# Kernel tuning notes

Measured on AMD Instinct MI355X. Metric: run time of the kernel, lower is better.

## Reference

```python
import jax, jax.numpy as jnp
import numpy as np

DIM = 2048
HEADS = 16
DIM_HEAD = 128
FF_MULT = 4
ATTN_INNER = HEADS * DIM_HEAD            # 2048
FF_INNER = DIM * FF_MULT                 # 8192
FUSED = ATTN_INNER + DIM_HEAD + DIM_HEAD + 2 * FF_INNER  # 18688
B, N = 2, 2048


def setup_inputs() -> dict:
    key = jax.random.key(0)
    k0, k1, k2, k3 = jax.random.split(key, 4)
    s = lambda fan_in: 1.0 / np.sqrt(fan_in)
    return {
        "x": jax.random.normal(k0, (B, N, DIM), jnp.float32),
        "gamma": jnp.ones((DIM,), jnp.float32),
        "beta": jnp.zeros((DIM,), jnp.float32),
        "w_fused": jax.random.normal(k1, (DIM, FUSED), jnp.float32) * s(DIM),
        "w_attn_out": jax.random.normal(k2, (ATTN_INNER, DIM), jnp.float32) * s(ATTN_INNER),
        "w_ff_out": jax.random.normal(k3, (FF_INNER, DIM), jnp.float32) * s(FF_INNER),
    }


def _rotate_half(t):
    t1, t2 = jnp.split(t, 2, axis=-1)
    return jnp.concatenate([-t2, t1], axis=-1)


def _rope(pos, t):
    # pos: [n, d] broadcast over leading dims of t (..., n, d)
    return t * jnp.cos(pos) + _rotate_half(t) * jnp.sin(pos)


def reference(x, gamma, beta, w_fused, w_attn_out, w_ff_out):
    b, n, d = x.shape
    # LayerNorm (eps = 1e-5, matching F.layer_norm default)
    mu = jnp.mean(x, axis=-1, keepdims=True)
    var = jnp.var(x, axis=-1, keepdims=True)
    h = (x - mu) * jax.lax.rsqrt(var + 1e-5) * gamma + beta

    # Fused projection feeding attention (multi-query) and parallel SwiGLU FF
    proj = h @ w_fused  # [b, n, FUSED]
    i0 = ATTN_INNER
    i1 = i0 + DIM_HEAD
    i2 = i1 + DIM_HEAD
    q, k, v, ff = jnp.split(proj, [i0, i1, i2], axis=-1)
    q = q.reshape(b, n, HEADS, DIM_HEAD).transpose(0, 2, 1, 3)  # [b, h, n, dh]

    # Rotary embedding: freqs duplicated, rotate-half application
    inv_freq = 1.0 / (10000.0 ** (jnp.arange(0, DIM_HEAD, 2, dtype=jnp.float32) / DIM_HEAD))
    freqs = jnp.arange(n, dtype=jnp.float32)[:, None] * inv_freq[None, :]
    pos = jnp.concatenate([freqs, freqs], axis=-1)  # [n, dh]
    q = _rope(pos, q)          # [b, h, n, dh]
    k = _rope(pos, k)          # [b, n, dh] (single KV head)

    # Multi-query causal attention
    scale = 1.0 / jnp.sqrt(jnp.asarray(DIM_HEAD, q.dtype))
    sim = jnp.einsum('bhid,bjd->bhij', q, k) * scale  # [b, h, n, n]
    causal = jnp.triu(jnp.ones((n, n), dtype=bool), 1)
    sim = jnp.where(causal, jnp.finfo(sim.dtype).min, sim)
    attn = jax.nn.softmax(sim, axis=-1)
    out = jnp.einsum('bhij,bjd->bhid', attn, v)       # [b, h, n, dh]
    out = out.transpose(0, 2, 1, 3).reshape(b, n, ATTN_INNER)

    # Parallel SwiGLU FF: chunk -> silu(gate) * x
    x_ff, gate = jnp.split(ff, 2, axis=-1)  # each [b, n, FF_INNER]
    ff_o = (jax.nn.silu(gate) * x_ff) @ w_ff_out

    return out @ w_attn_out + ff_o
```

## Files before the change

kernel.cpp:

```cpp
#include <hip/hip_runtime.h>
#include <hip/hip_bf16.h>
#include <math.h>

#define DIM 2048
#define HEADS 16
#define DH 128
#define ATTN_INNER 2048
#define FF_INNER 8192
#define FUSED_N 18688
#define QKV_N 2304
#define BATCH 2
#define SEQ 2048
#define ROWS (BATCH*SEQ)

typedef __attribute__((ext_vector_type(8))) __bf16 bf16x8;
typedef __attribute__((ext_vector_type(4))) float f32x4;
typedef __attribute__((ext_vector_type(16))) float f32x16;

typedef __attribute__((address_space(1))) void* as1_void;
typedef __attribute__((address_space(3))) void* as3_void;

__device__ __forceinline__ void async16(const void* g, void* l) {
  __builtin_amdgcn_global_load_lds((as1_void)const_cast<void*>(g), (as3_void)l, 16, 0, 0);
}

__global__ __launch_bounds__(256) void ln_kernel(const float* __restrict__ x,
                                                 const float* __restrict__ gamma,
                                                 const float* __restrict__ beta,
                                                 __hip_bfloat16* __restrict__ hb) {
  const int row = blockIdx.x;
  const int t = threadIdx.x;
  const float4* x4 = (const float4*)(x + (size_t)row * DIM);
  float4 a = x4[t];
  float4 c = x4[t + 256];
  float s  = a.x + a.y + a.z + a.w + c.x + c.y + c.z + c.w;
  float ss = a.x*a.x + a.y*a.y + a.z*a.z + a.w*a.w +
             c.x*c.x + c.y*c.y + c.z*c.z + c.w*c.w;
  for (int off = 32; off > 0; off >>= 1) {
    s  += __shfl_down(s, off);
    ss += __shfl_down(ss, off);
  }
  __shared__ float red[8];
  int wv = t >> 6, lane = t & 63;
  if (lane == 0) { red[wv] = s; red[wv + 4] = ss; }
  __syncthreads();
  s  = red[0] + red[1] + red[2] + red[3];
  ss = red[4] + red[5] + red[6] + red[7];
  float mu  = s * (1.0f / DIM);
  float var = ss * (1.0f / DIM) - mu * mu;
  float rs  = rsqrtf(var + 1e-5f);
  __hip_bfloat16* o = hb + (size_t)row * DIM;
  float v0[4] = {a.x, a.y, a.z, a.w};
  float v1[4] = {c.x, c.y, c.z, c.w};
#pragma unroll
  for (int i = 0; i < 4; i++) {
    int c0 = t * 4 + i;
    int c1 = 1024 + t * 4 + i;
    o[c0] = __float2bfloat16((v0[i] - mu) * rs * gamma[c0] + beta[c0]);
    o[c1] = __float2bfloat16((v1[i] - mu) * rs * gamma[c1] + beta[c1]);
  }
}

__global__ __launch_bounds__(256) void tcvt_kernel(const float* __restrict__ src,
                                                   __hip_bfloat16* __restrict__ dst,
                                                   int R, int C) {
  __shared__ float tile[64][65];
  const int cb = blockIdx.x * 64, rb = blockIdx.y * 64;
  const int t = threadIdx.x;
  const int lr = t >> 4, lc4 = (t & 15) * 4;
#pragma unroll
  for (int i = 0; i < 4; i++) {
    float4 v = *(const float4*)&src[(size_t)(rb + lr + i * 16) * C + cb + lc4];
    tile[lr + i * 16][lc4 + 0] = v.x;
    tile[lr + i * 16][lc4 + 1] = v.y;
    tile[lr + i * 16][lc4 + 2] = v.z;
    tile[lr + i * 16][lc4 + 3] = v.w;
  }
  __syncthreads();
  const int tcc = t & 31, trc = t >> 5;
#pragma unroll
  for (int i = 0; i < 8; i++) {
    int c = trc + i * 8;
    __hip_bfloat162 pk;
    pk.x = __float2bfloat16(tile[2 * tcc][c]);
    pk.y = __float2bfloat16(tile[2 * tcc + 1][c]);
    *(__hip_bfloat162*)&dst[(size_t)(cb + c) * R + rb + 2 * tcc] = pk;
  }
}

__global__ __launch_bounds__(256) void tbf16_kernel(const __hip_bfloat16* __restrict__ src, int lds_,
                                                    __hip_bfloat16* __restrict__ dst, int ldd,
                                                    int R, int C) {
  __shared__ __hip_bfloat16 tile[64][65];
  const int cb = blockIdx.x * 64, rb = blockIdx.y * 64;
  const int t = threadIdx.x;
  const int tc = t & 63, tr = t >> 6;
#pragma unroll
  for (int i = 0; i < 16; i++) {
    int r = tr + i * 4;
    tile[r][tc] = src[(size_t)(rb + r) * lds_ + cb + tc];
  }
  __syncthreads();
#pragma unroll
  for (int i = 0; i < 16; i++) {
    int c = tr + i * 4;
    dst[(size_t)(cb + c) * ldd + rb + tc] = tile[tc][c];
  }
}

__global__ __launch_bounds__(256) void rope_kernel(__hip_bfloat16* __restrict__ qkv) {
  const size_t tid = (size_t)blockIdx.x * 256 + threadIdx.x;
  const int d = tid & 63;
  const int u = (tid >> 6) % 17;
  const int row = tid / (17 * 64);
  const int n = row & (SEQ - 1);
  size_t base = (size_t)row * QKV_N + (u < 16 ? u * DH : ATTN_INNER);
  float inv = powf(10000.0f, -(float)d * (1.0f / 64.0f));
  float th = (float)n * inv;
  float cs = cosf(th), sn = sinf(th);
  float a = __bfloat162float(qkv[base + d]);
  float b = __bfloat162float(qkv[base + d + 64]);
  qkv[base + d]      = __float2bfloat16(a * cs - b * sn);
  qkv[base + d + 64] = __float2bfloat16(b * cs + a * sn);
}

__global__ __launch_bounds__(256, 3) void gemm_qkv(const __hip_bfloat16* __restrict__ A,
                                                   const __hip_bfloat16* __restrict__ Bt,
                                                   __hip_bfloat16* __restrict__ C) {
  __shared__ __hip_bfloat16 As[2][128 * 32];
  __shared__ __hip_bfloat16 Bs[2][128 * 32];
  const int tid = threadIdx.x;
  const int wv = tid >> 6, lane = tid & 63;
  const int l31 = lane & 31, khalf = lane >> 5;
  const int pid = blockIdx.x;
  const int gid = pid / 144, rem = pid % 144;
  const int m0 = (gid * 8 + (rem % 8)) * 128;
  const int n0 = (rem / 8) * 128;
  const int wm = (wv >> 1) * 64, wn = (wv & 1) * 64;
  const int srow = lane >> 2, scol = (lane & 3) * 8;

  f32x16 acc[2][2] = {};
  for (int k0 = 0; k0 < DIM; k0 += 64) {
#pragma unroll
    for (int h = 0; h < 2; h++)
#pragma unroll
      for (int j = 0; j < 2; j++) {
        int q = wv * 2 + j;
        int row = q * 16 + srow;
        async16(A  + (size_t)(m0 + row) * DIM + k0 + h * 32 + scol, &As[h][q * 512]);
        async16(Bt + (size_t)(n0 + row) * DIM + k0 + h * 32 + scol, &Bs[h][q * 512]);
      }
    __syncthreads();
#pragma unroll
    for (int h = 0; h < 2; h++)
#pragma unroll
      for (int kk = 0; kk < 2; kk++) {
        bf16x8 af[2], bfr[2];
#pragma unroll
        for (int i = 0; i < 2; i++)
          af[i] = *(const bf16x8*)(&As[h][(wm + i * 32 + l31) * 32 + kk * 16 + khalf * 8]);
#pragma unroll
        for (int j = 0; j < 2; j++)
          bfr[j] = *(const bf16x8*)(&Bs[h][(wn + j * 32 + l31) * 32 + kk * 16 + khalf * 8]);
#pragma unroll
        for (int i = 0; i < 2; i++)
#pragma unroll
          for (int j = 0; j < 2; j++)
            acc[i][j] = __builtin_amdgcn_mfma_f32_32x32x16_bf16(af[i], bfr[j], acc[i][j], 0, 0, 0);
      }
    __syncthreads();
  }
#pragma unroll
  for (int i = 0; i < 2; i++)
#pragma unroll
    for (int j = 0; j < 2; j++) {
      int colg = n0 + wn + j * 32 + l31;
#pragma unroll
      for (int r = 0; r < 16; r++) {
        int rowg = m0 + wm + i * 32 + (r & 3) + 4 * khalf + 8 * (r >> 2);
        C[(size_t)rowg * QKV_N + colg] = __float2bfloat16(acc[i][j][r]);
      }
    }
}

__global__ __launch_bounds__(256, 3) void gemm_ff(const __hip_bfloat16* __restrict__ A,
                                                  const __hip_bfloat16* __restrict__ W,
                                                  __hip_bfloat16* __restrict__ G) {
  __shared__ __hip_bfloat16 As[2][128 * 32];
  __shared__ __hip_bfloat16 Bs[2][128 * 32];
  const int tid = threadIdx.x;
  const int wv = tid >> 6, lane = tid & 63;
  const int l31 = lane & 31, khalf = lane >> 5;
  const int pid = blockIdx.x;
  const int xcd = pid & 7, lid = pid >> 3;
  const int m0 = (lid >> 4) * 128;
  const int n0 = (xcd * 16 + (lid & 15)) * 64;
  const int wm = (wv >> 1) * 64, wn2 = (wv & 1) * 32;
  const int srow = lane >> 2, scol = (lane & 3) * 8;

  f32x16 ax[2] = {};
  f32x16 ag[2] = {};
  for (int k0 = 0; k0 < DIM; k0 += 64) {
#pragma unroll
    for (int h = 0; h < 2; h++)
#pragma unroll
      for (int j = 0; j < 2; j++) {
        int q = wv * 2 + j;
        int row = q * 16 + srow;
        async16(A + (size_t)(m0 + row) * DIM + k0 + h * 32 + scol, &As[h][q * 512]);
        int wr = (row < 64) ? (QKV_N + n0 + row)
                            : (QKV_N + FF_INNER + n0 + row - 64);
        async16(W + (size_t)wr * DIM + k0 + h * 32 + scol, &Bs[h][q * 512]);
      }
    __syncthreads();
#pragma unroll
    for (int h = 0; h < 2; h++)
#pragma unroll
      for (int kk = 0; kk < 2; kk++) {
        bf16x8 af[2], bx, bg;
#pragma unroll
        for (int i = 0; i < 2; i++)
          af[i] = *(const bf16x8*)(&As[h][(wm + i * 32 + l31) * 32 + kk * 16 + khalf * 8]);
        bx = *(const bf16x8*)(&Bs[h][(wn2 + l31) * 32 + kk * 16 + khalf * 8]);
        bg = *(const bf16x8*)(&Bs[h][(64 + wn2 + l31) * 32 + kk * 16 + khalf * 8]);
#pragma unroll
        for (int i = 0; i < 2; i++) {
          ax[i] = __builtin_amdgcn_mfma_f32_32x32x16_bf16(af[i], bx, ax[i], 0, 0, 0);
          ag[i] = __builtin_amdgcn_mfma_f32_32x32x16_bf16(af[i], bg, ag[i], 0, 0, 0);
        }
      }
    __syncthreads();
  }
#pragma unroll
  for (int i = 0; i < 2; i++) {
    int colg = n0 + wn2 + l31;
#pragma unroll
    for (int r = 0; r < 16; r++) {
      int rowg = m0 + wm + i * 32 + (r & 3) + 4 * khalf + 8 * (r >> 2);
      float xv = ax[i][r];
      float gv = ag[i][r];
      float o = gv / (1.0f + expf(-gv)) * xv;
      G[(size_t)rowg * FF_INNER + colg] = __float2bfloat16(o);
    }
  }
}

__global__ __launch_bounds__(256, 3) void gemm_out(const __hip_bfloat16* __restrict__ A0,
                                                   const __hip_bfloat16* __restrict__ B0,
                                                   const __hip_bfloat16* __restrict__ A1,
                                                   const __hip_bfloat16* __restrict__ B1,
                                                   float* __restrict__ C) {
  __shared__ __hip_bfloat16 As[2][128 * 32];
  __shared__ __hip_bfloat16 Bs[2][128 * 32];
  const int tid = threadIdx.x;
  const int wv = tid >> 6, lane = tid & 63;
  const int l31 = lane & 31, khalf = lane >> 5;
  const int pid = blockIdx.x;
  const int xcd = pid & 7, lid = pid >> 3;
  const int m0 = ((xcd & 3) * 8 + (lid & 7)) * 128;
  const int n0 = ((xcd >> 2) * 8 + (lid >> 3)) * 128;
  const int wm = (wv >> 1) * 64, wn = (wv & 1) * 64;
  const int srow = lane >> 2, scol = (lane & 3) * 8;

  f32x16 acc[2][2] = {};
  for (int p = 0; p < 2; p++) {
    const __hip_bfloat16* A = p ? A1 : A0;
    const __hip_bfloat16* B = p ? B1 : B0;
    const int K = p ? FF_INNER : ATTN_INNER;
    for (int k0 = 0; k0 < K; k0 += 64) {
#pragma unroll
      for (int h = 0; h < 2; h++)
#pragma unroll
        for (int j = 0; j < 2; j++) {
          int q = wv * 2 + j;
          int row = q * 16 + srow;
          async16(A + (size_t)(m0 + row) * K + k0 + h * 32 + scol, &As[h][q * 512]);
          async16(B + (size_t)(n0 + row) * K + k0 + h * 32 + scol, &Bs[h][q * 512]);
        }
      __syncthreads();
#pragma unroll
      for (int h = 0; h < 2; h++)
#pragma unroll
        for (int kk = 0; kk < 2; kk++) {
          bf16x8 af[2], bfr[2];
#pragma unroll
          for (int i = 0; i < 2; i++)
            af[i] = *(const bf16x8*)(&As[h][(wm + i * 32 + l31) * 32 + kk * 16 + khalf * 8]);
#pragma unroll
          for (int j = 0; j < 2; j++)
            bfr[j] = *(const bf16x8*)(&Bs[h][(wn + j * 32 + l31) * 32 + kk * 16 + khalf * 8]);
#pragma unroll
          for (int i = 0; i < 2; i++)
#pragma unroll
            for (int j = 0; j < 2; j++)
              acc[i][j] = __builtin_amdgcn_mfma_f32_32x32x16_bf16(af[i], bfr[j], acc[i][j], 0, 0, 0);
        }
      __syncthreads();
    }
  }
#pragma unroll
  for (int i = 0; i < 2; i++)
#pragma unroll
    for (int j = 0; j < 2; j++) {
      int colg = n0 + wn + j * 32 + l31;
#pragma unroll
      for (int r = 0; r < 16; r++) {
        int rowg = m0 + wm + i * 32 + (r & 3) + 4 * khalf + 8 * (r >> 2);
        C[(size_t)rowg * DIM + colg] = acc[i][j][r];
      }
    }
}

__global__ __launch_bounds__(256) void flash_kernel(const __hip_bfloat16* __restrict__ qkv,
                                                    const __hip_bfloat16* __restrict__ vt,
                                                    __hip_bfloat16* __restrict__ aob) {
  __shared__ __hip_bfloat16 Qs[128 * 128];
  __shared__ __hip_bfloat16 Ks[64 * 128];
  __shared__ __hip_bfloat16 Vts[128 * 64];
  __shared__ __hip_bfloat16 Ps[128 * 64];

  const int blk = blockIdx.x;
  const int bh = blk & 31;
  const int qi = blk >> 5;
  const int qt = (qi & 1) ? (qi >> 1) : (15 - (qi >> 1));
  const int bat = bh >> 4, h = bh & 15;

  const int tid = threadIdx.x;
  const int wv = tid >> 6, lane = tid & 63;
  const int quad = lane >> 4, l15 = lane & 15;
  const float scale = 0.08838834764831845f;

#pragma unroll
  for (int j = 0; j < 8; j++) {
    int is = wv * 8 + j;
    int e = is * 512 + lane * 8;
    int r = e >> 7, c = e & 127;
    async16(qkv + (size_t)(bat * SEQ + qt * 128 + r) * QKV_N + h * DH + c, Qs + is * 512);
  }

  f32x4 oacc[2][8];
#pragma unroll
  for (int i = 0; i < 2; i++)
#pragma unroll
    for (int j = 0; j < 8; j++) oacc[i][j] = (f32x4){0.f, 0.f, 0.f, 0.f};
  float mrow[2][4], lrow[2][4];
#pragma unroll
  for (int i = 0; i < 2; i++)
#pragma unroll
    for (int r = 0; r < 4; r++) { mrow[i][r] = -INFINITY; lrow[i][r] = 0.f; }

  const int jt_max = 2 * qt + 1;
  for (int jt = 0; jt <= jt_max; jt++) {
    __syncthreads();
#pragma unroll
    for (int j = 0; j < 4; j++) {
      int is = wv * 4 + j;
      int e = is * 512 + lane * 8;
      { int r = e >> 7, c = e & 127;
        async16(qkv + (size_t)(bat * SEQ + jt * 64 + r) * QKV_N + ATTN_INNER + c, Ks + is * 512); }
      { int d = e >> 6, jc = e & 63;
        async16(vt + (size_t)d * ROWS + bat * SEQ + jt * 64 + jc, Vts + is * 512); }
    }
    __syncthreads();

    f32x4 sacc[2][4];
#pragma unroll
    for (int i = 0; i < 2; i++)
#pragma unroll
      for (int j = 0; j < 4; j++) sacc[i][j] = (f32x4){0.f, 0.f, 0.f, 0.f};
#pragma unroll
    for (int kq = 0; kq < 4; kq++) {
      bf16x8 qa[2], kb[4];
#pragma unroll
      for (int i = 0; i < 2; i++)
        qa[i] = *(const bf16x8*)(Qs + (wv * 32 + i * 16 + l15) * 128 + kq * 32 + quad * 8);
#pragma unroll
      for (int j = 0; j < 4; j++)
        kb[j] = *(const bf16x8*)(Ks + (j * 16 + l15) * 128 + kq * 32 + quad * 8);
#pragma unroll
      for (int i = 0; i < 2; i++)
#pragma unroll
        for (int j = 0; j < 4; j++)
          sacc[i][j] = __builtin_amdgcn_mfma_f32_16x16x32_bf16(qa[i], kb[j], sacc[i][j], 0, 0, 0);
    }

#pragma unroll
    for (int i = 0; i < 2; i++) {
#pragma unroll
      for (int r = 0; r < 4; r++) {
        int row_g = qt * 128 + wv * 32 + i * 16 + quad * 4 + r;
        float mt = -INFINITY;
#pragma unroll
        for (int j = 0; j < 4; j++) {
          int col_g = jt * 64 + j * 16 + l15;
          float sv = sacc[i][j][r] * scale;
          if (col_g > row_g) sv = -INFINITY;
          sacc[i][j][r] = sv;
          mt = fmaxf(mt, sv);
        }
#pragma unroll
        for (int off = 1; off < 16; off <<= 1) mt = fmaxf(mt, __shfl_xor(mt, off));
        float mn = fmaxf(mrow[i][r], mt);
        float al = expf(mrow[i][r] - mn);
        float rs = 0.f;
#pragma unroll
        for (int j = 0; j < 4; j++) {
          float p = expf(sacc[i][j][r] - mn);
          sacc[i][j][r] = p;
          rs += p;
        }
#pragma unroll
        for (int off = 1; off < 16; off <<= 1) rs += __shfl_xor(rs, off);
        lrow[i][r] = lrow[i][r] * al + rs;
        mrow[i][r] = mn;
#pragma unroll
        for (int i2 = 0; i2 < 8; i2++) oacc[i][i2][r] *= al;
      }
    }

#pragma unroll
    for (int i = 0; i < 2; i++)
#pragma unroll
      for (int j = 0; j < 4; j++)
#pragma unroll
        for (int r = 0; r < 4; r++)
          Ps[(wv * 32 + i * 16 + quad * 4 + r) * 64 + j * 16 + l15] =
              __float2bfloat16(sacc[i][j][r]);
    __syncthreads();

#pragma unroll
    for (int kp = 0; kp < 2; kp++) {
      bf16x8 pa[2], vb[8];
#pragma unroll
      for (int i = 0; i < 2; i++)
        pa[i] = *(const bf16x8*)(Ps + (wv * 32 + i * 16 + l15) * 64 + kp * 32 + quad * 8);
#pragma unroll
      for (int i2 = 0; i2 < 8; i2++)
        vb[i2] = *(const bf16x8*)(Vts + (i2 * 16 + l15) * 64 + kp * 32 + quad * 8);
#pragma unroll
      for (int i = 0; i < 2; i++)
#pragma unroll
        for (int i2 = 0; i2 < 8; i2++)
          oacc[i][i2] = __builtin_amdgcn_mfma_f32_16x16x32_bf16(pa[i], vb[i2], oacc[i][i2], 0, 0, 0);
    }
  }

#pragma unroll
  for (int i = 0; i < 2; i++)
#pragma unroll
    for (int r = 0; r < 4; r++) {
      float inv = 1.0f / lrow[i][r];
      int row_g = bat * SEQ + qt * 128 + wv * 32 + i * 16 + quad * 4 + r;
#pragma unroll
      for (int i2 = 0; i2 < 8; i2++)
        aob[(size_t)row_g * ATTN_INNER + h * DH + i2 * 16 + l15] =
            __float2bfloat16(oacc[i][i2][r] * inv);
    }
}

extern "C" void kernel_launch(void* const* d_in, const int* in_sizes, int n_in,
                              void* d_out, int out_size, void* d_ws, size_t ws_size,
                              hipStream_t stream) {
  const float* x       = (const float*)d_in[0];
  const float* gamma   = (const float*)d_in[1];
  const float* beta    = (const float*)d_in[2];
  const float* w_fused = (const float*)d_in[3];
  const float* w_attn  = (const float*)d_in[4];
  const float* w_ff    = (const float*)d_in[5];
  float* out = (float*)d_out;
  char* ws = (char*)d_ws;

  size_t off = 0;
  auto alloc = [&](size_t bytes) {
    size_t o = off;
    off += (bytes + 255) & ~(size_t)255;
    return o;
  };
  __hip_bfloat16* hb   = (__hip_bfloat16*)(ws + alloc((size_t)ROWS * DIM * 2));
  __hip_bfloat16* wfbt = (__hip_bfloat16*)(ws + alloc((size_t)FUSED_N * DIM * 2));
  __hip_bfloat16* qkvb = (__hip_bfloat16*)(ws + alloc((size_t)ROWS * QKV_N * 2));
  __hip_bfloat16* gb   = (__hip_bfloat16*)(ws + alloc((size_t)ROWS * FF_INNER * 2));
  __hip_bfloat16* wat  = (__hip_bfloat16*)(ws + alloc((size_t)DIM * ATTN_INNER * 2));
  __hip_bfloat16* wfot = (__hip_bfloat16*)(ws + alloc((size_t)DIM * FF_INNER * 2));
  __hip_bfloat16* vt   = (__hip_bfloat16*)(ws + alloc((size_t)DH * ROWS * 2));
  __hip_bfloat16* aob  = (__hip_bfloat16*)(ws + alloc((size_t)ROWS * ATTN_INNER * 2));

  ln_kernel<<<ROWS, 256, 0, stream>>>(x, gamma, beta, hb);

  tcvt_kernel<<<dim3(FUSED_N / 64, DIM / 64), 256, 0, stream>>>(w_fused, wfbt, DIM, FUSED_N);
  tcvt_kernel<<<dim3(DIM / 64, ATTN_INNER / 64), 256, 0, stream>>>(w_attn, wat, ATTN_INNER, DIM);
  tcvt_kernel<<<dim3(DIM / 64, FF_INNER / 64), 256, 0, stream>>>(w_ff, wfot, FF_INNER, DIM);

  gemm_qkv<<<(QKV_N / 128) * (ROWS / 128), 256, 0, stream>>>(hb, wfbt, qkvb);

  rope_kernel<<<(ROWS * 17 * 64) / 256, 256, 0, stream>>>(qkvb);

  tbf16_kernel<<<dim3(DH / 64, ROWS / 64), 256, 0, stream>>>(qkvb + ATTN_INNER + DH, QKV_N, vt, ROWS, ROWS, DH);

  flash_kernel<<<512, 256, 0, stream>>>(qkvb, vt, aob);

  gemm_ff<<<(FF_INNER / 64) * (ROWS / 128), 256, 0, stream>>>(hb, wfbt, gb);

  gemm_out<<<(DIM / 128) * (ROWS / 128), 256, 0, stream>>>(aob, wat, gb, wfot, out);

  (void)in_sizes; (void)n_in; (void)out_size; (void)ws_size;
}
```

Measured before the change: 1.191 ms.

## XOR-swizzle LDS tiles and remap GEMM block-to-XCD tile assignment

```diff
diff --git a/kernel.cpp b/kernel.cpp
--- a/kernel.cpp
+++ b/kernel.cpp
@@ -124,6 +124,7 @@
   qkv[base + d + 64] = __float2bfloat16(b * cs + a * sn);
 }
 
+
 __global__ __launch_bounds__(256, 3) void gemm_qkv(const __hip_bfloat16* __restrict__ A,
                                                    const __hip_bfloat16* __restrict__ Bt,
                                                    __hip_bfloat16* __restrict__ C) {
@@ -132,12 +133,14 @@
   const int tid = threadIdx.x;
   const int wv = tid >> 6, lane = tid & 63;
   const int l31 = lane & 31, khalf = lane >> 5;
+  const int rx = l31 & 3;
   const int pid = blockIdx.x;
-  const int gid = pid / 144, rem = pid % 144;
-  const int m0 = (gid * 8 + (rem % 8)) * 128;
-  const int n0 = (rem / 8) * 128;
+  const int xcd = pid & 7, lid = pid >> 3;
+  const int m0 = (xcd * 4 + (lid & 3)) * 128;
+  const int n0 = (lid >> 2) * 128;
   const int wm = (wv >> 1) * 64, wn = (wv & 1) * 64;
-  const int srow = lane >> 2, scol = (lane & 3) * 8;
+  const int srow = lane >> 2;
+  const int scol = (((lane & 3) ^ (srow & 3)) * 8);
 
   f32x16 acc[2][2] = {};
   for (int k0 = 0; k0 < DIM; k0 += 64) {
@@ -155,13 +158,14 @@
     for (int h = 0; h < 2; h++)
 #pragma unroll
       for (int kk = 0; kk < 2; kk++) {
+        const int blk = (kk * 2 + khalf) ^ rx;
         bf16x8 af[2], bfr[2];
 #pragma unroll
         for (int i = 0; i < 2; i++)
-          af[i] = *(const bf16x8*)(&As[h][(wm + i * 32 + l31) * 32 + kk * 16 + khalf * 8]);
+          af[i] = *(const bf16x8*)(&As[h][(wm + i * 32 + l31) * 32 + blk * 8]);
 #pragma unroll
         for (int j = 0; j < 2; j++)
-          bfr[j] = *(const bf16x8*)(&Bs[h][(wn + j * 32 + l31) * 32 + kk * 16 + khalf * 8]);
+          bfr[j] = *(const bf16x8*)(&Bs[h][(wn + j * 32 + l31) * 32 + blk * 8]);
 #pragma unroll
         for (int i = 0; i < 2; i++)
 #pragma unroll
@@ -191,12 +195,14 @@
   const int tid = threadIdx.x;
   const int wv = tid >> 6, lane = tid & 63;
   const int l31 = lane & 31, khalf = lane >> 5;
+  const int rx = l31 & 3;
   const int pid = blockIdx.x;
   const int xcd = pid & 7, lid = pid >> 3;
-  const int m0 = (lid >> 4) * 128;
-  const int n0 = (xcd * 16 + (lid & 15)) * 64;
+  const int m0 = (xcd * 4 + (lid & 3)) * 128;
+  const int n0 = (lid >> 2) * 64;
   const int wm = (wv >> 1) * 64, wn2 = (wv & 1) * 32;
-  const int srow = lane >> 2, scol = (lane & 3) * 8;
+  const int srow = lane >> 2;
+  const int scol = (((lane & 3) ^ (srow & 3)) * 8);
 
   f32x16 ax[2] = {};
   f32x16 ag[2] = {};
@@ -217,12 +223,13 @@
     for (int h = 0; h < 2; h++)
 #pragma unroll
       for (int kk = 0; kk < 2; kk++) {
+        const int blk = (kk * 2 + khalf) ^ rx;
         bf16x8 af[2], bx, bg;
 #pragma unroll
         for (int i = 0; i < 2; i++)
-          af[i] = *(const bf16x8*)(&As[h][(wm + i * 32 + l31) * 32 + kk * 16 + khalf * 8]);
-        bx = *(const bf16x8*)(&Bs[h][(wn2 + l31) * 32 + kk * 16 + khalf * 8]);
-        bg = *(const bf16x8*)(&Bs[h][(64 + wn2 + l31) * 32 + kk * 16 + khalf * 8]);
+          af[i] = *(const bf16x8*)(&As[h][(wm + i * 32 + l31) * 32 + blk * 8]);
+        bx = *(const bf16x8*)(&Bs[h][(wn2 + l31) * 32 + blk * 8]);
+        bg = *(const bf16x8*)(&Bs[h][(64 + wn2 + l31) * 32 + blk * 8]);
 #pragma unroll
         for (int i = 0; i < 2; i++) {
           ax[i] = __builtin_amdgcn_mfma_f32_32x32x16_bf16(af[i], bx, ax[i], 0, 0, 0);
@@ -255,12 +262,14 @@
   const int tid = threadIdx.x;
   const int wv = tid >> 6, lane = tid & 63;
   const int l31 = lane & 31, khalf = lane >> 5;
+  const int rx = l31 & 3;
   const int pid = blockIdx.x;
   const int xcd = pid & 7, lid = pid >> 3;
-  const int m0 = ((xcd & 3) * 8 + (lid & 7)) * 128;
-  const int n0 = ((xcd >> 2) * 8 + (lid >> 3)) * 128;
+  const int m0 = (xcd * 4 + (lid & 3)) * 128;
+  const int n0 = (lid >> 2) * 128;
   const int wm = (wv >> 1) * 64, wn = (wv & 1) * 64;
-  const int srow = lane >> 2, scol = (lane & 3) * 8;
+  const int srow = lane >> 2;
+  const int scol = (((lane & 3) ^ (srow & 3)) * 8);
 
   f32x16 acc[2][2] = {};
   for (int p = 0; p < 2; p++) {
@@ -282,13 +291,14 @@
       for (int h = 0; h < 2; h++)
 #pragma unroll
         for (int kk = 0; kk < 2; kk++) {
+          const int blk = (kk * 2 + khalf) ^ rx;
           bf16x8 af[2], bfr[2];
 #pragma unroll
           for (int i = 0; i < 2; i++)
-            af[i] = *(const bf16x8*)(&As[h][(wm + i * 32 + l31) * 32 + kk * 16 + khalf * 8]);
+            af[i] = *(const bf16x8*)(&As[h][(wm + i * 32 + l31) * 32 + blk * 8]);
 #pragma unroll
           for (int j = 0; j < 2; j++)
-            bfr[j] = *(const bf16x8*)(&Bs[h][(wn + j * 32 + l31) * 32 + kk * 16 + khalf * 8]);
+            bfr[j] = *(const bf16x8*)(&Bs[h][(wn + j * 32 + l31) * 32 + blk * 8]);
 #pragma unroll
           for (int i = 0; i < 2; i++)
 #pragma unroll
```

Measured after the change: 1.153 ms. 3.2% less time.
